# Optimization experiments

Measured on AMD Instinct MI355X. Metric: run time of the kernel, lower is better.

## Reference

```python
import jax, jax.numpy as jnp
import numpy as np

B, R, C, OUT, IN = 256, 1152, 10, 16, 8


def setup_inputs() -> dict:
    key = jax.random.key(0)
    kx, kw = jax.random.split(key)
    x = jax.random.normal(kx, (B, R, IN), dtype=jnp.float32)
    W = jax.random.normal(kw, (R, C, OUT, IN), dtype=jnp.float32)
    return {"x": x, "W": W}


def _squash(s):
    # s: [B, C, OUT]
    mag_sq = jnp.sum(s * s, axis=-1, keepdims=True)
    mag = jnp.sqrt(mag_sq + 1e-8)
    return mag_sq / (1.0 + mag_sq) * (s / (mag + 1e-8))


def reference(x, W):
    # u_hat[b,r,c,o] = sum_i W[r,c,o,i] * x[b,r,i]  (no explicit W.repeat)
    u_hat = jnp.einsum('rcoi,bri->brco', W, x)
    b_ij = jnp.zeros((B, R, C), dtype=u_hat.dtype)
    v_j = None
    for it in range(3):
        c_ij = jax.nn.softmax(b_ij, axis=2)              # [B,R,C]
        s_j = jnp.einsum('brc,brco->bco', c_ij, u_hat)   # [B,C,OUT]
        v_j = _squash(s_j)                               # [B,C,OUT]
        if it < 2:
            b_ij = b_ij + jnp.einsum('brco,bco->brc', u_hat, v_j)
    return v_j
```

## Files before the change

kernel.cpp:

```cpp
#include <hip/hip_runtime.h>
#include <math.h>


typedef _Float16 h2 __attribute__((ext_vector_type(2)));
typedef _Float16 h4 __attribute__((ext_vector_type(4)));

#if __has_builtin(__builtin_amdgcn_fdot2)
#define FDOT2(a, b, c) __builtin_amdgcn_fdot2((a), (b), (c), false)
#else
static __device__ __forceinline__ float FDOT2(h2 a, h2 b, float c) {
    return c + (float)a.x * (float)b.x + (float)a.y * (float)b.y;
}
#endif

#if __has_builtin(__builtin_amdgcn_rcpf)
#define FRCP(x) __builtin_amdgcn_rcpf(x)
#else
#define FRCP(x) (1.0f / (x))
#endif

#define BCH2(u) __builtin_bit_cast(h2, (u))

namespace {
constexpr int Bdim = 256;
constexpr int Rdim = 1152;
constexpr int Cdim = 10;
constexpr int Odim = 16;
constexpr int Idim = 8;
constexpr int CO   = 160;

constexpr int NRC   = 64;
constexpr int RPC   = 18;
constexpr int NPAIR = 9;
constexpr int NSP   = 16;
constexpr int WROW  = Cdim * Odim * Idim;
constexpr int REDP  = 162;
}

__global__ __launch_bounds__(256)
void conv_wx(const float* __restrict__ W, const float* __restrict__ x,
             _Float16* __restrict__ W16, _Float16* __restrict__ X16)
{
    constexpr int NW4 = Rdim * Cdim * Odim * Idim / 4;
    constexpr int NX4 = Bdim * Rdim * Idim / 4;
    const int i = blockIdx.x * 256 + threadIdx.x;
    if (i < NW4) {
        const float4 v = reinterpret_cast<const float4*>(W)[i];
        h4 o = { (_Float16)v.x, (_Float16)v.y, (_Float16)v.z, (_Float16)v.w };
        reinterpret_cast<h4*>(W16)[i] = o;
    } else if (i < NW4 + NX4) {
        const int j = i - NW4;
        const float4 v = reinterpret_cast<const float4*>(x)[j];
        h4 o = { (_Float16)v.x, (_Float16)v.y, (_Float16)v.z, (_Float16)v.w };
        reinterpret_cast<h4*>(X16)[j] = o;
    }
}

__device__ __forceinline__ void stagepair(const _Float16* __restrict__ src,
                                          _Float16* dst, int lane)
{
#pragma unroll
    for (int k = 0; k < 5; ++k) {
        const _Float16* s = src + (size_t)(k * 64 + lane) * 8;
        _Float16* d = dst + k * 512;
        __builtin_amdgcn_global_load_lds((const __attribute__((address_space(1))) void*)s,
                                         (__attribute__((address_space(3))) void*)d,
                                         16, 0, 0);
    }
}

template<bool FIRST>
__global__ __launch_bounds__(256)
void caps_iter(const _Float16* __restrict__ X16, const _Float16* __restrict__ W16,
               const float* __restrict__ Vsum, float* __restrict__ s_part)
{
    __shared__ _Float16 Wstage[4][2][2560];

    const int tid  = threadIdx.x;
    const int wv   = tid >> 6;
    const int lane = tid & 63;
    const int og   = lane & 7;
    const int bl   = lane >> 3;

    const int bgroup = blockIdx.x;
    const int rcq    = blockIdx.y;
    const int r0     = (rcq * 4 + wv) * RPC;
    const int b      = bgroup * 8 + bl;

    float va[Cdim], vb[Cdim];
    if constexpr (!FIRST) {
#pragma unroll
        for (int c = 0; c < Cdim; ++c) {
            const float2 vv = *reinterpret_cast<const float2*>(
                Vsum + (size_t)b * CO + c * Odim + og * 2);
            va[c] = vv.x; vb[c] = vv.y;
        }
    }

    float s0[Cdim], s1[Cdim];
#pragma unroll
    for (int c = 0; c < Cdim; ++c) { s0[c] = 0.f; s1[c] = 0.f; }

    const _Float16* Wr = W16 + (size_t)r0 * WROW;
    _Float16* const st0 = &Wstage[wv][0][0];
    _Float16* const st1 = &Wstage[wv][1][0];

    stagepair(Wr, st0, lane);
    uint4 xc0, xc1;
    {
        const uint4* xp = reinterpret_cast<const uint4*>(
            X16 + ((size_t)b * Rdim + r0) * Idim);
        xc0 = xp[0]; xc1 = xp[1];
    }

    for (int p = 0; p < NPAIR; ++p) {
        asm volatile("s_waitcnt vmcnt(0)" ::: "memory");

        const _Float16* stcur = (p & 1) ? st1 : st0;
        _Float16* stnxt = (p & 1) ? st0 : st1;
        uint4 xn0, xn1;
        if (p + 1 < NPAIR) {
            stagepair(Wr + (size_t)(p + 1) * 2560, stnxt, lane);
            const uint4* xq = reinterpret_cast<const uint4*>(
                X16 + ((size_t)b * Rdim + r0 + (p + 1) * 2) * Idim);
            xn0 = xq[0]; xn1 = xq[1];
        }

#pragma unroll
        for (int rl = 0; rl < 2; ++rl) {
            const uint4 xv = rl ? xc1 : xc0;
            const h2 x0 = BCH2(xv.x), x1 = BCH2(xv.y), x2 = BCH2(xv.z), x3 = BCH2(xv.w);

            float u0[Cdim], u1[Cdim];
#pragma unroll
            for (int c = 0; c < Cdim; ++c) {
                const uint4* wp = reinterpret_cast<const uint4*>(
                    stcur + rl * WROW + (c * Odim + og * 2) * Idim);
                const uint4 w0 = wp[0], w1 = wp[1];
                float a = FDOT2(BCH2(w0.x), x0, 0.f);
                a = FDOT2(BCH2(w0.y), x1, a);
                a = FDOT2(BCH2(w0.z), x2, a);
                u0[c] = FDOT2(BCH2(w0.w), x3, a);
                float d = FDOT2(BCH2(w1.x), x0, 0.f);
                d = FDOT2(BCH2(w1.y), x1, d);
                d = FDOT2(BCH2(w1.z), x2, d);
                u1[c] = FDOT2(BCH2(w1.w), x3, d);
            }

            if constexpr (FIRST) {
#pragma unroll
                for (int c = 0; c < Cdim; ++c) {
                    s0[c] += 0.1f * u0[c];
                    s1[c] += 0.1f * u1[c];
                }
            } else {
                float e[Cdim];
                float sum = 0.f;
#pragma unroll
                for (int c = 0; c < Cdim; ++c) {
                    float l = u0[c] * va[c] + u1[c] * vb[c];
                    l += __shfl_xor(l, 1);
                    l += __shfl_xor(l, 2);
                    l += __shfl_xor(l, 4);
                    e[c] = __expf(l);
                    sum += e[c];
                }
                const float rinv = FRCP(sum);
#pragma unroll
                for (int c = 0; c < Cdim; ++c) {
                    const float cw = e[c] * rinv;
                    s0[c] += cw * u0[c];
                    s1[c] += cw * u1[c];
                }
            }
        }

        if (p + 1 < NPAIR) { xc0 = xn0; xc1 = xn1; }
    }

    __syncthreads();
    float* red = reinterpret_cast<float*>(&Wstage[0][0][0]);
    {
        float* myrow = red + (wv * 8 + bl) * REDP + og * 2;
#pragma unroll
        for (int c = 0; c < Cdim; ++c)
            *reinterpret_cast<float2*>(myrow + c * Odim) = make_float2(s0[c], s1[c]);
    }
    __syncthreads();
#pragma unroll
    for (int k = 0; k < 5; ++k) {
        const int j  = k * 256 + tid;
        const int b2 = j / CO;
        const int co = j - b2 * CO;
        const int o  = b2 * REDP + co;
        const float t = red[o] + red[8 * REDP + o]
                      + red[16 * REDP + o] + red[24 * REDP + o];
        s_part[((size_t)rcq * Bdim + bgroup * 8 + b2) * CO + co] = t;
    }
}

template<int MODE>
__global__ __launch_bounds__(256)
void caps_reduce(const float* __restrict__ s_part, float* __restrict__ Vsum,
                 float* __restrict__ out)
{
    const int idx = blockIdx.x * 256 + threadIdx.x;
    float s = 0.f;
#pragma unroll
    for (int k = 0; k < NSP; ++k) s += s_part[(size_t)k * (Bdim * CO) + idx];

    float ssq = s * s;
    ssq += __shfl_xor(ssq, 1);
    ssq += __shfl_xor(ssq, 2);
    ssq += __shfl_xor(ssq, 4);
    ssq += __shfl_xor(ssq, 8);

    const float mag = sqrtf(ssq + 1e-8f);
    const float v = ssq / (1.f + ssq) * s / (mag + 1e-8f);

    if constexpr (MODE == 2) out[idx] = v;
    else if constexpr (MODE == 1) Vsum[idx] += v;
    else Vsum[idx] = v;
}

extern "C" void kernel_launch(void* const* d_in, const int* in_sizes, int n_in,
                              void* d_out, int out_size, void* d_ws, size_t ws_size,
                              hipStream_t stream)
{
    const float* x = (const float*)d_in[0];
    const float* W = (const float*)d_in[1];
    float* out = (float*)d_out;

    float* s_part = (float*)d_ws;
    float* Vsum   = s_part + (size_t)NSP * Bdim * CO;
    _Float16* W16 = (_Float16*)(Vsum + Bdim * CO);
    _Float16* X16 = W16 + (size_t)Rdim * Cdim * Odim * Idim;

    conv_wx<<<dim3(3744), dim3(256), 0, stream>>>(W, x, W16, X16);

    const dim3 gi(Bdim / 8, NSP);
    const dim3 bi(256);
    const dim3 gr((Bdim * CO) / 256);
    const dim3 br(256);

    caps_iter<true><<<gi, bi, 0, stream>>>(X16, W16, Vsum, s_part);
    caps_reduce<0><<<gr, br, 0, stream>>>(s_part, Vsum, out);
    caps_iter<false><<<gi, bi, 0, stream>>>(X16, W16, Vsum, s_part);
    caps_reduce<1><<<gr, br, 0, stream>>>(s_part, Vsum, out);
    caps_iter<false><<<gi, bi, 0, stream>>>(X16, W16, Vsum, s_part);
    caps_reduce<2><<<gr, br, 0, stream>>>(s_part, Vsum, out);
}
```

Before: 91.02 us.

## Split routing R dimension into 128 padded chunks with per-wave partial outputs

R is padded from 1152 to 1280 with zeroed W and x rows, so each wave can own a 10-row chunk. This doubles the iteration grid to 1024 blocks. Each wave now writes its own partial s directly to global memory, which removes the shared-memory reduction and the two block barriers. The aim is more parallelism and latency hiding. The cost is about 11% wasted compute on padded rows, a shorter double-buffer pipeline per wave, and an 8x larger partial buffer (128 slices instead of 16) that the reduce kernels must write and then read on every iteration.

```diff
diff --git a/kernel.cpp b/kernel.cpp
--- a/kernel.cpp
+++ b/kernel.cpp
@@ -29,29 +29,39 @@
 constexpr int Idim = 8;
 constexpr int CO   = 160;
 
-constexpr int NRC   = 64;
-constexpr int RPC   = 18;
-constexpr int NPAIR = 9;
-constexpr int NSP   = 16;
+constexpr int Rpad  = 1280;
+constexpr int RPC   = 10;
+constexpr int NPAIR = 5;
+constexpr int NCH   = 128;
 constexpr int WROW  = Cdim * Odim * Idim;
-constexpr int REDP  = 162;
 }
 
 __global__ __launch_bounds__(256)
 void conv_wx(const float* __restrict__ W, const float* __restrict__ x,
              _Float16* __restrict__ W16, _Float16* __restrict__ X16)
 {
-    constexpr int NW4 = Rdim * Cdim * Odim * Idim / 4;
-    constexpr int NX4 = Bdim * Rdim * Idim / 4;
+    constexpr int NW4 = Rpad * WROW / 4;
+    constexpr int NX4 = Bdim * Rpad * Idim / 4;
     const int i = blockIdx.x * 256 + threadIdx.x;
     if (i < NW4) {
-        const float4 v = reinterpret_cast<const float4*>(W)[i];
-        h4 o = { (_Float16)v.x, (_Float16)v.y, (_Float16)v.z, (_Float16)v.w };
+        const int r = i / (WROW / 4);
+        h4 o = { (_Float16)0.f, (_Float16)0.f, (_Float16)0.f, (_Float16)0.f };
+        if (r < Rdim) {
+            const float4 v = reinterpret_cast<const float4*>(W)[i];
+            o = { (_Float16)v.x, (_Float16)v.y, (_Float16)v.z, (_Float16)v.w };
+        }
         reinterpret_cast<h4*>(W16)[i] = o;
     } else if (i < NW4 + NX4) {
-        const int j = i - NW4;
-        const float4 v = reinterpret_cast<const float4*>(x)[j];
-        h4 o = { (_Float16)v.x, (_Float16)v.y, (_Float16)v.z, (_Float16)v.w };
+        const int j   = i - NW4;
+        const int b   = j / (Rpad * 2);
+        const int rem = j - b * (Rpad * 2);
+        const int r   = rem >> 1;
+        h4 o = { (_Float16)0.f, (_Float16)0.f, (_Float16)0.f, (_Float16)0.f };
+        if (r < Rdim) {
+            const float4 v = reinterpret_cast<const float4*>(x)
+                [((size_t)b * Rdim + r) * 2 + (rem & 1)];
+            o = { (_Float16)v.x, (_Float16)v.y, (_Float16)v.z, (_Float16)v.w };
+        }
         reinterpret_cast<h4*>(X16)[j] = o;
     }
 }
@@ -83,8 +93,8 @@
     const int bl   = lane >> 3;
 
     const int bgroup = blockIdx.x;
-    const int rcq    = blockIdx.y;
-    const int r0     = (rcq * 4 + wv) * RPC;
+    const int chunk  = blockIdx.y * 4 + wv;
+    const int r0     = chunk * RPC;
     const int b      = bgroup * 8 + bl;
 
     float va[Cdim], vb[Cdim];
@@ -109,7 +119,7 @@
     uint4 xc0, xc1;
     {
         const uint4* xp = reinterpret_cast<const uint4*>(
-            X16 + ((size_t)b * Rdim + r0) * Idim);
+            X16 + ((size_t)b * Rpad + r0) * Idim);
         xc0 = xp[0]; xc1 = xp[1];
     }
 
@@ -122,7 +132,7 @@
         if (p + 1 < NPAIR) {
             stagepair(Wr + (size_t)(p + 1) * 2560, stnxt, lane);
             const uint4* xq = reinterpret_cast<const uint4*>(
-                X16 + ((size_t)b * Rdim + r0 + (p + 1) * 2) * Idim);
+                X16 + ((size_t)b * Rpad + r0 + (p + 1) * 2) * Idim);
             xn0 = xq[0]; xn1 = xq[1];
         }
 
@@ -178,25 +188,10 @@
         if (p + 1 < NPAIR) { xc0 = xn0; xc1 = xn1; }
     }
 
-    __syncthreads();
-    float* red = reinterpret_cast<float*>(&Wstage[0][0][0]);
-    {
-        float* myrow = red + (wv * 8 + bl) * REDP + og * 2;
-#pragma unroll
-        for (int c = 0; c < Cdim; ++c)
-            *reinterpret_cast<float2*>(myrow + c * Odim) = make_float2(s0[c], s1[c]);
-    }
-    __syncthreads();
-#pragma unroll
-    for (int k = 0; k < 5; ++k) {
-        const int j  = k * 256 + tid;
-        const int b2 = j / CO;
-        const int co = j - b2 * CO;
-        const int o  = b2 * REDP + co;
-        const float t = red[o] + red[8 * REDP + o]
-                      + red[16 * REDP + o] + red[24 * REDP + o];
-        s_part[((size_t)rcq * Bdim + bgroup * 8 + b2) * CO + co] = t;
-    }
+    float* dst = s_part + ((size_t)chunk * Bdim + b) * CO + og * 2;
+#pragma unroll
+    for (int c = 0; c < Cdim; ++c)
+        *reinterpret_cast<float2*>(dst + c * Odim) = make_float2(s0[c], s1[c]);
 }
 
 template<int MODE>
@@ -206,8 +201,8 @@
 {
     const int idx = blockIdx.x * 256 + threadIdx.x;
     float s = 0.f;
-#pragma unroll
-    for (int k = 0; k < NSP; ++k) s += s_part[(size_t)k * (Bdim * CO) + idx];
+#pragma unroll 8
+    for (int k = 0; k < NCH; ++k) s += s_part[(size_t)k * (Bdim * CO) + idx];
 
     float ssq = s * s;
     ssq += __shfl_xor(ssq, 1);
@@ -232,13 +227,13 @@
     float* out = (float*)d_out;
 
     float* s_part = (float*)d_ws;
-    float* Vsum   = s_part + (size_t)NSP * Bdim * CO;
+    float* Vsum   = s_part + (size_t)NCH * Bdim * CO;
     _Float16* W16 = (_Float16*)(Vsum + Bdim * CO);
-    _Float16* X16 = W16 + (size_t)Rdim * Cdim * Odim * Idim;
-
-    conv_wx<<<dim3(3744), dim3(256), 0, stream>>>(W, x, W16, X16);
-
-    const dim3 gi(Bdim / 8, NSP);
+    _Float16* X16 = W16 + (size_t)Rpad * WROW;
+
+    conv_wx<<<dim3(4160), dim3(256), 0, stream>>>(W, x, W16, X16);
+
+    const dim3 gi(Bdim / 8, NCH / 4);
     const dim3 bi(256);
     const dim3 gr((Bdim * CO) / 256);
     const dim3 br(256);
```

Result: slower. 106.8 us (+17.4%).
